# Performance work log

Hardware: AMD Instinct MI355X
Metric: run time of the kernel (lower is better)

Reference implementation:

```python
import jax, jax.numpy as jnp
import numpy as np

B, S, D = 4, 4096, 1024  # batch, seq_len, d_k == d_v (num_heads forced to 1 by module shapes)


def setup_inputs() -> dict:
    key = jax.random.key(0)
    ks = jax.random.split(key, 11)
    scale = 1.0 / np.sqrt(D).astype(np.float32)
    inp = {
        "query": jax.random.normal(ks[0], (B, S, D), dtype=jnp.float32),
        "key": jax.random.normal(ks[1], (B, S, D), dtype=jnp.float32),
        "value": jax.random.normal(ks[2], (B, S, D), dtype=jnp.float32),
        # torch Linear weights stored as [in, out] so y = x @ W + b
        "Wh": jax.random.normal(ks[3], (D, D), dtype=jnp.float32) * scale,  # head_weight
        "bh": jax.random.normal(ks[4], (D,), dtype=jnp.float32) * scale,
        "Wk": jax.random.normal(ks[5], (D, D), dtype=jnp.float32) * scale,  # key_weight
        "bk": jax.random.normal(ks[6], (D,), dtype=jnp.float32) * scale,
        "Wv": jax.random.normal(ks[7], (D, D), dtype=jnp.float32) * scale,  # value_weight
        "bv": jax.random.normal(ks[8], (D,), dtype=jnp.float32) * scale,
        "Wo": jax.random.normal(ks[9], (D, D), dtype=jnp.float32) * scale,  # output_weight
        "bo": jax.random.normal(ks[10], (D,), dtype=jnp.float32) * scale,
    }
    return inp


def reference(query, key, value, Wh, bh, Wk, bk, Wv, bv, Wo, bo):
    d_k = Wh.shape[0]
    # quirk of the original module: head_weight is applied to ALL of q, k, v first
    q = query @ Wh + bh                      # [B,S,D]
    k = (key @ Wh + bh) @ Wk + bk            # [B,S,D]
    v = (value @ Wh + bh) @ Wv + bv          # [B,S,D]
    # quirk: qk is scaled TWICE by 1/sqrt(d_k) -> total scale 1/d_k
    scores = jnp.einsum("bqd,bkd->bqk", q, k) / jnp.asarray(d_k, q.dtype)
    attn = jax.nn.softmax(scores, axis=-1)   # [B,S,S]; dropout_p=0 -> identity
    out = jnp.einsum("bqk,bkd->bqd", attn, v)  # [B,S,D]
    return out @ Wo + bo                     # [B,S,D]
```

## Files before the change

### kernel.cpp

```cpp
#include <hip/hip_runtime.h>
#include <stdint.h>

typedef __bf16 bf16x8 __attribute__((ext_vector_type(8)));
typedef float f32x4 __attribute__((ext_vector_type(4)));

__device__ __forceinline__ unsigned short f2b(float f) {
  unsigned int u = __builtin_bit_cast(unsigned int, f);
  u += 0x7fffu + ((u >> 16) & 1u);
  return (unsigned short)(u >> 16);
}
__device__ __forceinline__ float b2f(unsigned short h) {
  unsigned int u = ((unsigned int)h) << 16;
  return __builtin_bit_cast(float, u);
}
__device__ __forceinline__ unsigned short to_bits(float f) { return f2b(f); }
__device__ __forceinline__ unsigned short to_bits(unsigned short u) { return u; }

__device__ __forceinline__ void gl2lds16(const void* g, void* l) {
  __builtin_amdgcn_global_load_lds(
      (const __attribute__((address_space(1))) unsigned int*)g,
      (__attribute__((address_space(3))) unsigned int*)l, 16, 0, 0);
}

#define FENCE asm volatile("" ::: "memory")

template <int OUT_BF16, int HAS_BIAS>
__global__ __launch_bounds__(512, 2) void gemm_bt8(
    const unsigned short* __restrict__ A, const unsigned short* __restrict__ BT,
    const float* __restrict__ bias, void* __restrict__ Cv, int N, int K,
    float scale, long zA, long zB, long zC) {
  __shared__ __align__(16) unsigned short lds[2][2][2][256][32];

  const int t = threadIdx.x;
  const int lane = t & 63;
  const int w = t >> 6;
  const int wm = w >> 2;
  const int wn = w & 3;

  const int gx = gridDim.x, gy = gridDim.y;
  const int nxy = gx * gy;
  int id = (blockIdx.z * gy + blockIdx.y) * gx + blockIdx.x;
  const int nwg = nxy * gridDim.z;
  id = (id & 7) * (nwg >> 3) + (id >> 3);
  const int bz = id / nxy;
  const int rem = id - bz * nxy;
  const long tileM = (long)(rem / gx) * 256;
  const long tileN = (long)(rem % gx) * 256;

  const unsigned short* Ab = A + (long)bz * zA;
  const unsigned short* Bb = BT + (long)bz * zB;

  const int srow = w * 32 + (lane >> 2);
  const int skb = ((lane & 3) ^ ((lane >> 3) & 3)) * 8;
  const unsigned short* Asrc = Ab + (tileM + srow) * K + skb;
  const unsigned short* Bsrc = Bb + (tileN + srow) * K + skb;
  const long jstep = (long)16 * K;

#define STG(OP, SRC, BUF, KH, KT)                                           \
  do {                                                                      \
    gl2lds16((SRC) + (KT) + (KH) * 32, &lds[BUF][OP][KH][w * 32][0]);       \
    gl2lds16((SRC) + jstep + (KT) + (KH) * 32,                              \
             &lds[BUF][OP][KH][w * 32 + 16][0]);                            \
  } while (0)

  const int fr = lane & 15;
  const int fsw = ((lane >> 4) ^ ((lane >> 1) & 3)) * 8;

  f32x4 acc[8][4];
#pragma unroll
  for (int m = 0; m < 8; ++m)
#pragma unroll
    for (int n = 0; n < 4; ++n) acc[m][n] = (f32x4)(0.f);

#define PHASE(BUF, MH, KH, STAGES, WAITC)                                   \
  {                                                                         \
    bf16x8 fa[4], fb[4];                                                    \
    _Pragma("unroll") for (int i = 0; i < 4; ++i) fa[i] =                   \
        *(const bf16x8*)&lds[BUF][0][KH][wm * 128 + MH * 64 + i * 16 + fr][fsw]; \
    _Pragma("unroll") for (int i = 0; i < 4; ++i) fb[i] =                   \
        *(const bf16x8*)&lds[BUF][1][KH][wn * 64 + i * 16 + fr][fsw];       \
    STAGES;                                                                 \
    FENCE;                                                                  \
    __builtin_amdgcn_s_barrier();                                           \
    asm volatile("s_waitcnt lgkmcnt(0)" ::: "memory");                      \
    __builtin_amdgcn_s_setprio(1);                                          \
    _Pragma("unroll") for (int i = 0; i < 4; ++i)                           \
        _Pragma("unroll") for (int n = 0; n < 4; ++n) acc[MH * 4 + i][n] =  \
            __builtin_amdgcn_mfma_f32_16x16x32_bf16(fa[i], fb[n],           \
                                                    acc[MH * 4 + i][n], 0,  \
                                                    0, 0);                  \
    __builtin_amdgcn_s_setprio(0);                                          \
    WAITC;                                                                  \
    FENCE;                                                                  \
    __builtin_amdgcn_s_barrier();                                           \
    FENCE;                                                                  \
  }

  const int NT = K >> 6;

  STG(0, Asrc, 0, 0, 0);
  STG(1, Bsrc, 0, 0, 0);
  STG(0, Asrc, 0, 1, 0);
  STG(1, Bsrc, 0, 1, 0);
  STG(0, Asrc, 1, 0, 64);
  STG(1, Bsrc, 1, 0, 64);
  asm volatile("s_waitcnt vmcnt(4)" ::: "memory");
  FENCE;
  __builtin_amdgcn_s_barrier();
  FENCE;

  for (int it = 0; it < NT; it += 2) {
    const int kt1 = (it + 1) << 6;
    const int kt2 = (it + 2) << 6;
    const int kt3 = (it + 3) << 6;
    const bool more = (it + 2) < NT;
    PHASE(0, 0, 0, { STG(0, Asrc, 1, 1, kt1); }, {});
    PHASE(0, 1, 0, { STG(1, Bsrc, 1, 1, kt1); }, {});
    PHASE(0, 0, 1, { if (more) STG(0, Asrc, 0, 0, kt2); }, {});
    PHASE(0, 1, 1, { if (more) STG(1, Bsrc, 0, 0, kt2); },
          {
            if (more)
              asm volatile("s_waitcnt vmcnt(4)" ::: "memory");
            else
              asm volatile("s_waitcnt vmcnt(0)" ::: "memory");
          });
    PHASE(1, 0, 0, { if (more) STG(0, Asrc, 0, 1, kt2); }, {});
    PHASE(1, 1, 0, { if (more) STG(1, Bsrc, 0, 1, kt2); }, {});
    PHASE(1, 0, 1, { if (more) STG(0, Asrc, 1, 0, kt3); }, {});
    PHASE(1, 1, 1, { if (more) STG(1, Bsrc, 1, 0, kt3); },
          {
            if (more)
              asm volatile("s_waitcnt vmcnt(4)" ::: "memory");
            else
              asm volatile("s_waitcnt vmcnt(0)" ::: "memory");
          });
  }
#undef PHASE
#undef STG

  const int cr = (lane >> 4) * 4;
  const int cc = lane & 15;
  char* Cb = (char*)Cv;
#pragma unroll
  for (int m = 0; m < 8; ++m) {
#pragma unroll
    for (int n = 0; n < 4; ++n) {
      const long col = tileN + wn * 64 + n * 16 + cc;
      const float bvv = HAS_BIAS ? bias[col] : 0.f;
#pragma unroll
      for (int j = 0; j < 4; ++j) {
        const long row = tileM + wm * 128 + m * 16 + cr + j;
        float v = acc[m][n][j] * scale + bvv;
        if (OUT_BF16)
          ((unsigned short*)Cb)[(long)bz * zC + row * N + col] = f2b(v);
        else
          ((float*)Cb)[(long)bz * zC + row * N + col] = v;
      }
    }
  }
}

template <int OUT_BF16, int HAS_BIAS>
__global__ __launch_bounds__(256, 2) void gemm_bt(
    const unsigned short* __restrict__ A, const unsigned short* __restrict__ BT,
    const float* __restrict__ bias, void* __restrict__ Cv, int M, int N, int K,
    float scale) {
  __shared__ __align__(16) unsigned short sA0[128 * 32];
  __shared__ __align__(16) unsigned short sB0[128 * 32];
  __shared__ __align__(16) unsigned short sA1[128 * 32];
  __shared__ __align__(16) unsigned short sB1[128 * 32];

  const int t = threadIdx.x;
  const int lane = t & 63;
  const int wave = t >> 6;
  const int wr = (wave >> 1) * 64;
  const int wc = (wave & 1) * 64;
  const long tileM = (long)blockIdx.y * 128;
  const long tileN = (long)blockIdx.x * 128;

  const int sr = t >> 2;
  const int sk = (t & 3) * 8;
  const unsigned short* Ap = A + (tileM + sr) * K + sk;
  const unsigned short* Bp = BT + (tileN + sr) * K + sk;
  const long rowstep = (long)64 * K;
  const int wo = wave * 512;

  f32x4 acc[4][4];
#pragma unroll
  for (int m = 0; m < 4; ++m)
#pragma unroll
    for (int n = 0; n < 4; ++n) acc[m][n] = (f32x4)(0.f);

  const int fr = lane & 15;
  const int fk = (lane >> 4) * 8;

#define STAGE(sa, sb, k0)                            \
  do {                                               \
    gl2lds16(Ap + (k0), (sa) + wo);                  \
    gl2lds16(Ap + rowstep + (k0), (sa) + 2048 + wo); \
    gl2lds16(Bp + (k0), (sb) + wo);                  \
    gl2lds16(Bp + rowstep + (k0), (sb) + 2048 + wo); \
  } while (0)

#define COMPUTE(sa, sb)                                                  \
  do {                                                                   \
    bf16x8 fa[4], fb[4];                                                 \
    _Pragma("unroll") for (int m = 0; m < 4; ++m) fa[m] =                \
        *(const bf16x8*)((sa) + (wr + m * 16 + fr) * 32 + fk);           \
    _Pragma("unroll") for (int n = 0; n < 4; ++n) fb[n] =                \
        *(const bf16x8*)((sb) + (wc + n * 16 + fr) * 32 + fk);           \
    _Pragma("unroll") for (int m = 0; m < 4; ++m)                        \
        _Pragma("unroll") for (int n = 0; n < 4; ++n) acc[m][n] =        \
            __builtin_amdgcn_mfma_f32_16x16x32_bf16(fa[m], fb[n],        \
                                                    acc[m][n], 0, 0, 0); \
  } while (0)

  const int nt = K >> 5;
  STAGE(sA0, sB0, 0);
  __syncthreads();
  for (int t2 = 0; t2 < nt; t2 += 2) {
    if (t2 + 1 < nt) STAGE(sA1, sB1, (t2 + 1) << 5);
    COMPUTE(sA0, sB0);
    __syncthreads();
    if (t2 + 2 < nt) STAGE(sA0, sB0, (t2 + 2) << 5);
    COMPUTE(sA1, sB1);
    __syncthreads();
  }
#undef STAGE
#undef COMPUTE

  const int cr = (lane >> 4) * 4;
  const int cc = lane & 15;
#pragma unroll
  for (int m = 0; m < 4; ++m) {
#pragma unroll
    for (int n = 0; n < 4; ++n) {
      const long col = tileN + wc + n * 16 + cc;
      const float bvv = HAS_BIAS ? bias[col] : 0.f;
#pragma unroll
      for (int j = 0; j < 4; ++j) {
        const long row = tileM + wr + m * 16 + cr + j;
        float v = acc[m][n][j] * scale + bvv;
        if (OUT_BF16)
          ((unsigned short*)Cv)[row * N + col] = f2b(v);
        else
          ((float*)Cv)[row * N + col] = v;
      }
    }
  }
}

__global__ __launch_bounds__(256) void softmax_rows(unsigned short* S,
                                                    int ncols) {
  const int t = threadIdx.x;
  const int lane = t & 63;
  const int wave = t >> 6;
  unsigned short* p = S + (long)blockIdx.x * ncols + t * 16;
  uint4 d0 = *(const uint4*)(p);
  uint4 d1 = *(const uint4*)(p + 8);
  unsigned int w[8] = {d0.x, d0.y, d0.z, d0.w, d1.x, d1.y, d1.z, d1.w};
  float v[16];
#pragma unroll
  for (int i = 0; i < 8; ++i) {
    v[2 * i] = b2f((unsigned short)(w[i] & 0xffffu));
    v[2 * i + 1] = b2f((unsigned short)(w[i] >> 16));
  }
  float mx = v[0];
#pragma unroll
  for (int i = 1; i < 16; ++i) mx = fmaxf(mx, v[i]);
#pragma unroll
  for (int off = 32; off > 0; off >>= 1) mx = fmaxf(mx, __shfl_xor(mx, off, 64));
  __shared__ float redm[4], reds[4];
  if (lane == 0) redm[wave] = mx;
  __syncthreads();
  mx = fmaxf(fmaxf(redm[0], redm[1]), fmaxf(redm[2], redm[3]));
  float sum = 0.f;
#pragma unroll
  for (int i = 0; i < 16; ++i) {
    v[i] = __expf(v[i] - mx);
    sum += v[i];
  }
#pragma unroll
  for (int off = 32; off > 0; off >>= 1) sum += __shfl_xor(sum, off, 64);
  if (lane == 0) reds[wave] = sum;
  __syncthreads();
  const float inv = 1.f / (reds[0] + reds[1] + reds[2] + reds[3]);
  unsigned int o[8];
#pragma unroll
  for (int i = 0; i < 8; ++i)
    o[i] = (unsigned int)f2b(v[2 * i] * inv) |
           ((unsigned int)f2b(v[2 * i + 1] * inv) << 16);
  *(uint4*)(p) = make_uint4(o[0], o[1], o[2], o[3]);
  *(uint4*)(p + 8) = make_uint4(o[4], o[5], o[6], o[7]);
}

template <typename TIN>
__global__ void transpose_cast(const TIN* __restrict__ in,
                               unsigned short* __restrict__ out, int R, int C) {
  __shared__ unsigned short tile[32][33];
  const long zoff = (long)blockIdx.z * R * C;
  in += zoff;
  out += zoff;
  const int tx = threadIdx.x, ty = threadIdx.y;
  const int bx = blockIdx.x * 32;
  const int by = blockIdx.y * 32;
#pragma unroll
  for (int i = 0; i < 4; ++i)
    tile[ty + i * 8][tx] = to_bits(in[(long)(by + ty + i * 8) * C + bx + tx]);
  __syncthreads();
#pragma unroll
  for (int i = 0; i < 4; ++i)
    out[(long)(bx + ty + i * 8) * R + by + tx] = tile[tx][ty + i * 8];
}

__global__ __launch_bounds__(256) void cast_f32_bf16(
    const float* __restrict__ in, unsigned short* __restrict__ out, long n) {
  long i = ((long)blockIdx.x * 256 + threadIdx.x) * 4;
  const long stride = (long)gridDim.x * 256 * 4;
  for (; i < n; i += stride) {
    float4 f = *(const float4*)(&in[i]);
    uint2 o;
    o.x = (unsigned int)f2b(f.x) | ((unsigned int)f2b(f.y) << 16);
    o.y = (unsigned int)f2b(f.z) | ((unsigned int)f2b(f.w) << 16);
    *(uint2*)(&out[i]) = o;
  }
}

extern "C" void kernel_launch(void* const* d_in, const int* in_sizes, int n_in,
                              void* d_out, int out_size, void* d_ws,
                              size_t ws_size, hipStream_t stream) {
  constexpr int Bb = 4, S = 4096, D = 1024;
  constexpr long SD = (long)S * D;
  constexpr long SS = (long)S * S;
  const float* query = (const float*)d_in[0];
  const float* key_ = (const float*)d_in[1];
  const float* value = (const float*)d_in[2];
  const float* Wh = (const float*)d_in[3];
  const float* bh = (const float*)d_in[4];
  const float* Wk = (const float*)d_in[5];
  const float* bk = (const float*)d_in[6];
  const float* Wv = (const float*)d_in[7];
  const float* bv = (const float*)d_in[8];
  const float* Wo = (const float*)d_in[9];
  const float* bo = (const float*)d_in[10];
  float* out = (float*)d_out;

  char* ws = (char*)d_ws;
  const long MB = 1024 * 1024;
  if (ws_size < (size_t)(232 * MB)) return;
  const bool batched = ws_size >= (size_t)(328 * MB);
  unsigned short* whT = (unsigned short*)(ws + 0 * MB);
  unsigned short* wkT = (unsigned short*)(ws + 2 * MB);
  unsigned short* wvT = (unsigned short*)(ws + 4 * MB);
  unsigned short* woT = (unsigned short*)(ws + 6 * MB);
  unsigned short* Xb = (unsigned short*)(ws + 8 * MB);
  unsigned short* q = (unsigned short*)(ws + 40 * MB);
  unsigned short* Kb = (unsigned short*)(ws + 72 * MB);
  unsigned short* Vb = (unsigned short*)(ws + 104 * MB);
  unsigned short* VT = (unsigned short*)(ws + 136 * MB);
  unsigned short* Hb = (unsigned short*)(ws + 168 * MB);
  unsigned short* Sc = (unsigned short*)(ws + 200 * MB);

  dim3 tb32(32, 8);
  transpose_cast<float><<<dim3(32, 32, 1), tb32, 0, stream>>>(Wh, whT, D, D);
  transpose_cast<float><<<dim3(32, 32, 1), tb32, 0, stream>>>(Wk, wkT, D, D);
  transpose_cast<float><<<dim3(32, 32, 1), tb32, 0, stream>>>(Wv, wvT, D, D);
  transpose_cast<float><<<dim3(32, 32, 1), tb32, 0, stream>>>(Wo, woT, D, D);

  const long nX = (long)Bb * SD;
  dim3 gProj(D / 256, Bb * S / 256, 1);

  cast_f32_bf16<<<2048, 256, 0, stream>>>(query, Xb, nX);
  gemm_bt8<1, 1><<<gProj, 512, 0, stream>>>(Xb, whT, bh, q, D, D, 1.f, 0, 0, 0);
  cast_f32_bf16<<<2048, 256, 0, stream>>>(key_, Xb, nX);
  gemm_bt8<1, 1><<<gProj, 512, 0, stream>>>(Xb, whT, bh, Hb, D, D, 1.f, 0, 0, 0);
  gemm_bt8<1, 1><<<gProj, 512, 0, stream>>>(Hb, wkT, bk, Kb, D, D, 1.f, 0, 0, 0);
  cast_f32_bf16<<<2048, 256, 0, stream>>>(value, Xb, nX);
  gemm_bt8<1, 1><<<gProj, 512, 0, stream>>>(Xb, whT, bh, Hb, D, D, 1.f, 0, 0, 0);
  gemm_bt8<1, 1><<<gProj, 512, 0, stream>>>(Hb, wvT, bv, Vb, D, D, 1.f, 0, 0, 0);

  transpose_cast<unsigned short>
      <<<dim3(D / 32, S / 32, Bb), tb32, 0, stream>>>(Vb, VT, S, D);

  const unsigned short* attn_out;
  if (batched) {
    gemm_bt8<1, 0><<<dim3(S / 256, S / 256, Bb), 512, 0, stream>>>(
        q, Kb, nullptr, Sc, S, D, 1.f / 1024.f, SD, SD, SS);
    softmax_rows<<<Bb * S, 256, 0, stream>>>(Sc, S);
    gemm_bt8<1, 0><<<dim3(D / 256, S / 256, Bb), 512, 0, stream>>>(
        Sc, VT, nullptr, q, D, S, 1.f, SS, SD, SD);
    attn_out = q;
  } else {
    for (int b = 0; b < Bb; ++b) {
      const unsigned short* qb = q + b * SD;
      const unsigned short* kb = Kb + b * SD;
      const unsigned short* vtb = VT + b * SD;
      unsigned short* ob = Vb + b * SD;
      gemm_bt8<1, 0><<<dim3(S / 256, S / 256, 1), 512, 0, stream>>>(
          qb, kb, nullptr, Sc, S, D, 1.f / 1024.f, 0, 0, 0);
      softmax_rows<<<S, 256, 0, stream>>>(Sc, S);
      gemm_bt<1, 0><<<dim3(D / 128, S / 128), 256, 0, stream>>>(
          Sc, vtb, nullptr, ob, S, D, S, 1.f);
    }
    attn_out = Vb;
  }

  gemm_bt8<0, 1><<<gProj, 512, 0, stream>>>(attn_out, woT, bo, out, D, D, 1.f,
                                            0, 0, 0);
}
```

Before: 937.1 us.

## Fold head weight into key/value weights and always use batched attention

Precomputes Wh@Wk and Wh@Wv, plus the matching fused biases, once in a small GEMM and a bias kernel. Key and value projections then each take one GEMM over the 16K-row activations instead of two, and the Hb intermediate is no longer written or read back. The workspace is repacked with aliased buffers so the batched attention path always fits, and the per-batch fallback and the old gemm_bt kernel are removed. The fused weights are rounded to bf16, which changes the rounding of the K and V projections slightly.

```diff
diff --git a/kernel.cpp b/kernel.cpp
--- a/kernel.cpp
+++ b/kernel.cpp
@@ -56,11 +56,11 @@
   const unsigned short* Bsrc = Bb + (tileN + srow) * K + skb;
   const long jstep = (long)16 * K;
 
-#define STG(OP, SRC, BUF, KH, KT)                                           \
-  do {                                                                      \
-    gl2lds16((SRC) + (KT) + (KH) * 32, &lds[BUF][OP][KH][w * 32][0]);       \
-    gl2lds16((SRC) + jstep + (KT) + (KH) * 32,                              \
-             &lds[BUF][OP][KH][w * 32 + 16][0]);                            \
+#define STG(OP, SRC, BUF, KH, KT)                                     \
+  do {                                                                \
+    gl2lds16((SRC) + (KT) + (KH) * 32, &lds[BUF][OP][KH][w * 32][0]); \
+    gl2lds16((SRC) + jstep + (KT) + (KH) * 32,                        \
+             &lds[BUF][OP][KH][w * 32 + 16][0]);                      \
   } while (0)
 
   const int fr = lane & 15;
@@ -160,94 +160,25 @@
   }
 }
 
-template <int OUT_BF16, int HAS_BIAS>
-__global__ __launch_bounds__(256, 2) void gemm_bt(
-    const unsigned short* __restrict__ A, const unsigned short* __restrict__ BT,
-    const float* __restrict__ bias, void* __restrict__ Cv, int M, int N, int K,
-    float scale) {
-  __shared__ __align__(16) unsigned short sA0[128 * 32];
-  __shared__ __align__(16) unsigned short sB0[128 * 32];
-  __shared__ __align__(16) unsigned short sA1[128 * 32];
-  __shared__ __align__(16) unsigned short sB1[128 * 32];
-
-  const int t = threadIdx.x;
-  const int lane = t & 63;
-  const int wave = t >> 6;
-  const int wr = (wave >> 1) * 64;
-  const int wc = (wave & 1) * 64;
-  const long tileM = (long)blockIdx.y * 128;
-  const long tileN = (long)blockIdx.x * 128;
-
-  const int sr = t >> 2;
-  const int sk = (t & 3) * 8;
-  const unsigned short* Ap = A + (tileM + sr) * K + sk;
-  const unsigned short* Bp = BT + (tileN + sr) * K + sk;
-  const long rowstep = (long)64 * K;
-  const int wo = wave * 512;
-
-  f32x4 acc[4][4];
-#pragma unroll
-  for (int m = 0; m < 4; ++m)
-#pragma unroll
-    for (int n = 0; n < 4; ++n) acc[m][n] = (f32x4)(0.f);
-
-  const int fr = lane & 15;
-  const int fk = (lane >> 4) * 8;
-
-#define STAGE(sa, sb, k0)                            \
-  do {                                               \
-    gl2lds16(Ap + (k0), (sa) + wo);                  \
-    gl2lds16(Ap + rowstep + (k0), (sa) + 2048 + wo); \
-    gl2lds16(Bp + (k0), (sb) + wo);                  \
-    gl2lds16(Bp + rowstep + (k0), (sb) + 2048 + wo); \
-  } while (0)
-
-#define COMPUTE(sa, sb)                                                  \
-  do {                                                                   \
-    bf16x8 fa[4], fb[4];                                                 \
-    _Pragma("unroll") for (int m = 0; m < 4; ++m) fa[m] =                \
-        *(const bf16x8*)((sa) + (wr + m * 16 + fr) * 32 + fk);           \
-    _Pragma("unroll") for (int n = 0; n < 4; ++n) fb[n] =                \
-        *(const bf16x8*)((sb) + (wc + n * 16 + fr) * 32 + fk);           \
-    _Pragma("unroll") for (int m = 0; m < 4; ++m)                        \
-        _Pragma("unroll") for (int n = 0; n < 4; ++n) acc[m][n] =        \
-            __builtin_amdgcn_mfma_f32_16x16x32_bf16(fa[m], fb[n],        \
-                                                    acc[m][n], 0, 0, 0); \
-  } while (0)
-
-  const int nt = K >> 5;
-  STAGE(sA0, sB0, 0);
-  __syncthreads();
-  for (int t2 = 0; t2 < nt; t2 += 2) {
-    if (t2 + 1 < nt) STAGE(sA1, sB1, (t2 + 1) << 5);
-    COMPUTE(sA0, sB0);
-    __syncthreads();
-    if (t2 + 2 < nt) STAGE(sA0, sB0, (t2 + 2) << 5);
-    COMPUTE(sA1, sB1);
-    __syncthreads();
-  }
-#undef STAGE
-#undef COMPUTE
-
-  const int cr = (lane >> 4) * 4;
-  const int cc = lane & 15;
-#pragma unroll
-  for (int m = 0; m < 4; ++m) {
-#pragma unroll
-    for (int n = 0; n < 4; ++n) {
-      const long col = tileN + wc + n * 16 + cc;
-      const float bvv = HAS_BIAS ? bias[col] : 0.f;
-#pragma unroll
-      for (int j = 0; j < 4; ++j) {
-        const long row = tileM + wr + m * 16 + cr + j;
-        float v = acc[m][n][j] * scale + bvv;
-        if (OUT_BF16)
-          ((unsigned short*)Cv)[row * N + col] = f2b(v);
-        else
-          ((float*)Cv)[row * N + col] = v;
-      }
-    }
-  }
+__global__ __launch_bounds__(64) void fused_bias2(
+    const unsigned short* __restrict__ wkT, const unsigned short* __restrict__ wvT,
+    const float* __restrict__ bh, const float* __restrict__ bk,
+    const float* __restrict__ bv, float* __restrict__ bhk,
+    float* __restrict__ bhv) {
+  const int n = blockIdx.x;
+  const unsigned short* wrow = (blockIdx.y == 0 ? wkT : wvT) + (long)n * 1024;
+  const float* badd = blockIdx.y == 0 ? bk : bv;
+  float* o = blockIdx.y == 0 ? bhk : bhv;
+  const int lane = threadIdx.x;
+  float s = 0.f;
+#pragma unroll
+  for (int i = 0; i < 16; ++i) {
+    const int d = lane + i * 64;
+    s += bh[d] * b2f(wrow[d]);
+  }
+#pragma unroll
+  for (int off = 32; off > 0; off >>= 1) s += __shfl_xor(s, off, 64);
+  if (lane == 0) o[n] = s + badd[n];
 }
 
 __global__ __launch_bounds__(256) void softmax_rows(unsigned short* S,
@@ -332,6 +263,7 @@
   constexpr int Bb = 4, S = 4096, D = 1024;
   constexpr long SD = (long)S * D;
   constexpr long SS = (long)S * S;
+  constexpr long DD = (long)D * D;
   const float* query = (const float*)d_in[0];
   const float* key_ = (const float*)d_in[1];
   const float* value = (const float*)d_in[2];
@@ -348,18 +280,21 @@
   char* ws = (char*)d_ws;
   const long MB = 1024 * 1024;
   if (ws_size < (size_t)(232 * MB)) return;
-  const bool batched = ws_size >= (size_t)(328 * MB);
   unsigned short* whT = (unsigned short*)(ws + 0 * MB);
   unsigned short* wkT = (unsigned short*)(ws + 2 * MB);
   unsigned short* wvT = (unsigned short*)(ws + 4 * MB);
   unsigned short* woT = (unsigned short*)(ws + 6 * MB);
-  unsigned short* Xb = (unsigned short*)(ws + 8 * MB);
-  unsigned short* q = (unsigned short*)(ws + 40 * MB);
-  unsigned short* Kb = (unsigned short*)(ws + 72 * MB);
-  unsigned short* Vb = (unsigned short*)(ws + 104 * MB);
-  unsigned short* VT = (unsigned short*)(ws + 136 * MB);
-  unsigned short* Hb = (unsigned short*)(ws + 168 * MB);
-  unsigned short* Sc = (unsigned short*)(ws + 200 * MB);
+  unsigned short* q = (unsigned short*)(ws + 8 * MB);
+  unsigned short* Kb = (unsigned short*)(ws + 40 * MB);
+  unsigned short* VT = (unsigned short*)(ws + 72 * MB);
+  unsigned short* Sc = (unsigned short*)(ws + 104 * MB);
+  unsigned short* Xb = (unsigned short*)(ws + 104 * MB);
+  unsigned short* Vb = (unsigned short*)(ws + 136 * MB);
+  unsigned short* WhB = (unsigned short*)(ws + 168 * MB);
+  unsigned short* FkT = (unsigned short*)(ws + 170 * MB);
+  unsigned short* FvT = (unsigned short*)(ws + 172 * MB);
+  float* bhk = (float*)(ws + 174 * MB);
+  float* bhv = (float*)(ws + 174 * MB + 4096);
 
   dim3 tb32(32, 8);
   transpose_cast<float><<<dim3(32, 32, 1), tb32, 0, stream>>>(Wh, whT, D, D);
@@ -367,44 +302,29 @@
   transpose_cast<float><<<dim3(32, 32, 1), tb32, 0, stream>>>(Wv, wvT, D, D);
   transpose_cast<float><<<dim3(32, 32, 1), tb32, 0, stream>>>(Wo, woT, D, D);
 
+  cast_f32_bf16<<<1024, 256, 0, stream>>>(Wh, WhB, DD);
+  gemm_bt8<1, 0><<<dim3(D / 256, D / 256, 2), 512, 0, stream>>>(
+      wkT, WhB, nullptr, FkT, D, D, 1.f, DD, 0, DD);
+  fused_bias2<<<dim3(D, 2), 64, 0, stream>>>(wkT, wvT, bh, bk, bv, bhk, bhv);
+
   const long nX = (long)Bb * SD;
   dim3 gProj(D / 256, Bb * S / 256, 1);
 
   cast_f32_bf16<<<2048, 256, 0, stream>>>(query, Xb, nX);
   gemm_bt8<1, 1><<<gProj, 512, 0, stream>>>(Xb, whT, bh, q, D, D, 1.f, 0, 0, 0);
   cast_f32_bf16<<<2048, 256, 0, stream>>>(key_, Xb, nX);
-  gemm_bt8<1, 1><<<gProj, 512, 0, stream>>>(Xb, whT, bh, Hb, D, D, 1.f, 0, 0, 0);
-  gemm_bt8<1, 1><<<gProj, 512, 0, stream>>>(Hb, wkT, bk, Kb, D, D, 1.f, 0, 0, 0);
+  gemm_bt8<1, 1><<<gProj, 512, 0, stream>>>(Xb, FkT, bhk, Kb, D, D, 1.f, 0, 0, 0);
   cast_f32_bf16<<<2048, 256, 0, stream>>>(value, Xb, nX);
-  gemm_bt8<1, 1><<<gProj, 512, 0, stream>>>(Xb, whT, bh, Hb, D, D, 1.f, 0, 0, 0);
-  gemm_bt8<1, 1><<<gProj, 512, 0, stream>>>(Hb, wvT, bv, Vb, D, D, 1.f, 0, 0, 0);
+  gemm_bt8<1, 1><<<gProj, 512, 0, stream>>>(Xb, FvT, bhv, Vb, D, D, 1.f, 0, 0, 0);
 
   transpose_cast<unsigned short>
       <<<dim3(D / 32, S / 32, Bb), tb32, 0, stream>>>(Vb, VT, S, D);
 
-  const unsigned short* attn_out;
-  if (batched) {
-    gemm_bt8<1, 0><<<dim3(S / 256, S / 256, Bb), 512, 0, stream>>>(
-        q, Kb, nullptr, Sc, S, D, 1.f / 1024.f, SD, SD, SS);
-    softmax_rows<<<Bb * S, 256, 0, stream>>>(Sc, S);
-    gemm_bt8<1, 0><<<dim3(D / 256, S / 256, Bb), 512, 0, stream>>>(
-        Sc, VT, nullptr, q, D, S, 1.f, SS, SD, SD);
-    attn_out = q;
-  } else {
-    for (int b = 0; b < Bb; ++b) {
-      const unsigned short* qb = q + b * SD;
-      const unsigned short* kb = Kb + b * SD;
-      const unsigned short* vtb = VT + b * SD;
-      unsigned short* ob = Vb + b * SD;
-      gemm_bt8<1, 0><<<dim3(S / 256, S / 256, 1), 512, 0, stream>>>(
-          qb, kb, nullptr, Sc, S, D, 1.f / 1024.f, 0, 0, 0);
-      softmax_rows<<<S, 256, 0, stream>>>(Sc, S);
-      gemm_bt<1, 0><<<dim3(D / 128, S / 128), 256, 0, stream>>>(
-          Sc, vtb, nullptr, ob, S, D, S, 1.f);
-    }
-    attn_out = Vb;
-  }
-
-  gemm_bt8<0, 1><<<gProj, 512, 0, stream>>>(attn_out, woT, bo, out, D, D, 1.f,
-                                            0, 0, 0);
-}
+  gemm_bt8<1, 0><<<dim3(S / 256, S / 256, Bb), 512, 0, stream>>>(
+      q, Kb, nullptr, Sc, S, D, 1.f / 1024.f, SD, SD, SS);
+  softmax_rows<<<Bb * S, 256, 0, stream>>>(Sc, S);
+  gemm_bt8<1, 0><<<dim3(D / 256, S / 256, Bb), 512, 0, stream>>>(
+      Sc, VT, nullptr, q, D, S, 1.f, SS, SD, SD);
+
+  gemm_bt8<0, 1><<<gProj, 512, 0, stream>>>(q, woT, bo, out, D, D, 1.f, 0, 0, 0);
+}
```

Result: faster. 755.4 us (-19.4%).
